# Kernel optimization log

Measured on AMD Instinct MI355X. Metric: run time of the kernel, lower is better.

Reference implementation:

```python
import jax, jax.numpy as jnp
import numpy as np
import math

DIM = 2880
N_HEADS = 64
N_KV = 8
HEAD_DIM = 64
WINDOW = 128          # layer_id = 0 (even) -> sliding window active
BASE = 150000.0
INIT_CTX = 4096
SCALE = 32.0
NTK_ALPHA = 1.0
NTK_BETA = 32.0
EPS = 1e-5
SEQ = 1536
BATCH = 1
SM_SCALE = 1.0 / math.sqrt(HEAD_DIM)


def _rope_tables(seq_len):
    """YaRN (NTK-by-parts) cos/sin tables, half-split convention. [S, D/2]."""
    freq = BASE ** (np.arange(0, HEAD_DIM, 2, dtype=np.float32) / HEAD_DIM)
    concentration = 0.1 * math.log(SCALE) + 1.0
    d_half = HEAD_DIM / 2
    low = d_half * math.log(INIT_CTX / (NTK_BETA * 2 * math.pi)) / math.log(BASE)
    high = d_half * math.log(INIT_CTX / (NTK_ALPHA * 2 * math.pi)) / math.log(BASE)
    interpolation = 1.0 / (SCALE * freq)
    extrapolation = 1.0 / freq
    ramp = (np.arange(d_half, dtype=np.float32) - low) / (high - low)
    mask = 1.0 - np.clip(ramp, 0.0, 1.0)
    inv_freq = interpolation * (1.0 - mask) + extrapolation * mask
    t = np.arange(seq_len, dtype=np.float32)
    freqs = np.outer(t, inv_freq)
    return (jnp.asarray(np.cos(freqs) * concentration),
            jnp.asarray(np.sin(freqs) * concentration))


def _apply_rope(x, cos, sin):
    # x: [B, S, H, D]; cos/sin: [S, D/2]
    c = cos[None, :, None, :]
    s = sin[None, :, None, :]
    x1, x2 = jnp.split(x, 2, axis=-1)
    return jnp.concatenate([x1 * c - x2 * s, x2 * c + x1 * s], axis=-1)


def setup_inputs() -> dict:
    key = jax.random.key(0)
    ks = jax.random.split(key, 5)
    x = jax.random.normal(ks[0], (BATCH, SEQ, DIM), dtype=jnp.float32)
    sinks = jax.random.normal(ks[1], (N_HEADS,), dtype=jnp.float32)
    norm_w = jnp.ones((DIM,), dtype=jnp.float32)
    qkv_dim = HEAD_DIM * (N_HEADS + 2 * N_KV)  # 5120
    qkv_w = jax.random.normal(ks[2], (qkv_dim, DIM), dtype=jnp.float32) / math.sqrt(DIM)
    qkv_b = jnp.zeros((qkv_dim,), dtype=jnp.float32)
    out_w = jax.random.normal(ks[3], (DIM, N_HEADS * HEAD_DIM), dtype=jnp.float32) / math.sqrt(N_HEADS * HEAD_DIM)
    out_b = jnp.zeros((DIM,), dtype=jnp.float32)
    return {"x": x, "sinks": sinks, "norm_w": norm_w, "qkv_w": qkv_w,
            "qkv_b": qkv_b, "out_w": out_w, "out_b": out_b}


def reference(x, sinks, norm_w, qkv_w, qkv_b, out_w, out_b):
    B, S, _ = x.shape
    # RMSNorm
    t = x * jax.lax.rsqrt(jnp.mean(x * x, axis=-1, keepdims=True) + EPS) * norm_w
    # fused QKV projection
    qkv = t @ qkv_w.T + qkv_b
    q_dim = N_HEADS * HEAD_DIM
    kv_dim = N_KV * HEAD_DIM
    q = qkv[..., :q_dim].reshape(B, S, N_HEADS, HEAD_DIM)
    k = qkv[..., q_dim:q_dim + kv_dim].reshape(B, S, N_KV, HEAD_DIM)
    v = qkv[..., q_dim + kv_dim:].reshape(B, S, N_KV, HEAD_DIM)
    # YaRN RoPE
    cos, sin = _rope_tables(S)
    q = _apply_rope(q, cos, sin)
    k = _apply_rope(k, cos, sin)
    # GQA: group query heads per kv head
    G = N_HEADS // N_KV
    qg = q.reshape(B, S, N_KV, G, HEAD_DIM)
    scores = jnp.einsum('bqkgd,bskd->bkgqs', qg, k) * SM_SCALE  # [B,KV,G,Sq,Sk]
    # causal + sliding-window mask
    i = jnp.arange(S)[:, None]
    j = jnp.arange(S)[None, :]
    allowed = j <= i
    if WINDOW > 0:
        allowed = allowed & ((i - j) < WINDOW)
    scores = jnp.where(allowed, scores, -jnp.inf)
    # sink tokens: one extra learned logit per head in the softmax denominator
    sink = sinks.reshape(N_KV, G)[None, :, :, None, None]
    sink = jnp.broadcast_to(sink, (B, N_KV, G, S, 1))
    logits = jnp.concatenate([scores, sink], axis=-1)  # [B,KV,G,Sq,Sk+1]
    p = jax.nn.softmax(logits, axis=-1)[..., :S]        # drop sink column
    attn = jnp.einsum('bkgqs,bskd->bqkgd', p, v).reshape(B, S, N_HEADS * HEAD_DIM)
    return attn @ out_w.T + out_b
```

## Files before the change

kernel.cpp:

```cpp
#include <hip/hip_runtime.h>

typedef unsigned short u16;
typedef unsigned int u32;
typedef __bf16 bf16x8 __attribute__((ext_vector_type(8)));
typedef float f32x4 __attribute__((ext_vector_type(4)));

#define S_LEN 1536
#define DIM 2880
#define NQH 64
#define NKVH 8
#define HD 64
#define QKV_N 5120
#define QDIM 4096
#define KVDIM 512
#define WIN 128
#define SM_SCALE 0.125f

__device__ __forceinline__ u16 f2bf(float f) {
  union { float f; u32 u; } a; a.f = f;
  u32 u = a.u;
  u32 lsb = (u >> 16) & 1;
  u += 0x7fffu + lsb;
  return (u16)(u >> 16);
}
__device__ __forceinline__ u32 pk2bf(float a, float b) {
  return (u32)f2bf(a) | ((u32)f2bf(b) << 16);
}

#define GLOAD16(g, l) __builtin_amdgcn_global_load_lds( \
    (const __attribute__((address_space(1))) u32*)(g), \
    (__attribute__((address_space(3))) u32*)(l), 16, 0, 0)

__global__ void rope_tables(float* __restrict__ cosT, float* __restrict__ sinT) {
  int idx = blockIdx.x * blockDim.x + threadIdx.x;
  if (idx >= S_LEN * 32) return;
  int s = idx >> 5, d = idx & 31;
  const double TWO_PI = 6.283185307179586;
  double freq = pow(150000.0, (double)d / 32.0);
  double conc = 0.1 * log(32.0) + 1.0;
  double lb = log(150000.0);
  double low = 32.0 * log(4096.0 / (32.0 * TWO_PI)) / lb;
  double high = 32.0 * log(4096.0 / (1.0 * TWO_PI)) / lb;
  double interp = 1.0 / (32.0 * freq), extra = 1.0 / freq;
  double ramp = ((double)d - low) / (high - low);
  ramp = ramp < 0.0 ? 0.0 : (ramp > 1.0 ? 1.0 : ramp);
  double maskv = 1.0 - ramp;
  double invf = interp * (1.0 - maskv) + extra * maskv;
  double ang = (double)s * invf;
  cosT[idx] = (float)(cos(ang) * conc);
  sinT[idx] = (float)(sin(ang) * conc);
}

__global__ __launch_bounds__(256) void rmsnorm_bf16(
    const float* __restrict__ x, const float* __restrict__ wgt,
    u16* __restrict__ th) {
  int row = blockIdx.x;
  const float* xr = x + (size_t)row * DIM;
  float ss = 0.f;
  for (int i = threadIdx.x; i < DIM / 4; i += 256) {
    float4 v = *(const float4*)&xr[i * 4];
    ss += v.x * v.x + v.y * v.y + v.z * v.z + v.w * v.w;
  }
  for (int m = 32; m >= 1; m >>= 1) ss += __shfl_xor(ss, m);
  __shared__ float red[4];
  int lane = threadIdx.x & 63, w = threadIdx.x >> 6;
  if (lane == 0) red[w] = ss;
  __syncthreads();
  float tot = red[0] + red[1] + red[2] + red[3];
  float scale = rsqrtf(tot / (float)DIM + 1e-5f);
  for (int i = threadIdx.x; i < DIM / 4; i += 256) {
    float4 v = *(const float4*)&xr[i * 4];
    float4 g = *(const float4*)&wgt[i * 4];
    ushort4 hi;
    hi.x = f2bf(v.x * scale * g.x);
    hi.y = f2bf(v.y * scale * g.y);
    hi.z = f2bf(v.z * scale * g.z);
    hi.w = f2bf(v.w * scale * g.w);
    *(ushort4*)&th[(size_t)row * DIM + i * 4] = hi;
  }
}

__global__ __launch_bounds__(256) void conv2(
    const float* __restrict__ s1, u16* __restrict__ d1, long n1,
    const float* __restrict__ s2, u16* __restrict__ d2, long n2) {
  long idx = (long)blockIdx.x * 256 + threadIdx.x;
  const float* src; u16* dst; long i;
  if (idx < n1) { src = s1; dst = d1; i = idx; }
  else if (idx < n1 + n2) { src = s2; dst = d2; i = idx - n1; }
  else return;
  float4 v = *(const float4*)&src[i * 4];
  ushort4 h;
  h.x = f2bf(v.x); h.y = f2bf(v.y); h.z = f2bf(v.z); h.w = f2bf(v.w);
  *(ushort4*)&dst[i * 4] = h;
}


__global__ __launch_bounds__(256) void gemm_rope(
    const u16* __restrict__ A, const u16* __restrict__ B,
    const float* __restrict__ bias,
    const float* __restrict__ cosT, const float* __restrict__ sinT,
    u16* __restrict__ Qb, u16* __restrict__ Kb, u16* __restrict__ Vt) {
  __shared__ u16 As[3 * 2048];
  __shared__ u16 Bs[3 * 4096];
  const int K = DIM;
  const int t = threadIdx.x;
  const int lane = t & 63, w = t >> 6;

  const int nby = gridDim.y;
  const int nwg = gridDim.x * nby;
  int orig = blockIdx.x * nby + blockIdx.y;
  {
    int q = nwg >> 3, r = nwg & 7;
    int xcd = orig & 7, i = orig >> 3;
    orig = (xcd < r ? xcd * (q + 1) : r * (q + 1) + (xcd - r) * q) + i;
  }
  const int m0 = (orig % nby) * 64, n0 = (orig / nby) * 128;

  const int wr = (w >> 1) * 32, wc = (w & 1) * 64;
  const int lr = lane & 15, lk8 = (lane >> 4) * 8;
  const int g4 = (lane >> 4) * 4;
  f32x4 acc[2][4] = {};

  const size_t ga  = (size_t)(m0 + (t >> 2)) * K + ((t & 3) * 8);
  const size_t gb0 = (size_t)(n0 + (t >> 2)) * K + ((t & 3) * 8);
  const size_t gb1 = (size_t)(n0 + 64 + (t >> 2)) * K + ((t & 3) * 8);
  const int la = t * 8, lb0 = t * 8, lb1 = (t + 256) * 8;

  auto STAGE = [&](int buf, int k0) {
    GLOAD16(A + ga + k0, &As[buf * 2048 + la]);
    GLOAD16(B + gb0 + k0, &Bs[buf * 4096 + lb0]);
    GLOAD16(B + gb1 + k0, &Bs[buf * 4096 + lb1]);
  };

  const int nk = K / 32;
  STAGE(0, 0); STAGE(1, 32);

  for (int tt = 0; tt < nk; ++tt) {
    const int cur = tt % 3;
    if (tt + 2 < nk) {
      STAGE((tt + 2) % 3, (tt + 2) * 32);
      asm volatile("s_waitcnt vmcnt(6)" ::: "memory");
    } else if (tt + 1 < nk) {
      asm volatile("s_waitcnt vmcnt(3)" ::: "memory");
    } else {
      asm volatile("s_waitcnt vmcnt(0)" ::: "memory");
    }
    __builtin_amdgcn_s_barrier();
    __builtin_amdgcn_sched_barrier(0);
    const u16* as_ = &As[cur * 2048];
    const u16* bs_ = &Bs[cur * 4096];
    bf16x8 af[2], bf_[4];
#pragma unroll
    for (int i = 0; i < 2; ++i) af[i] = *(const bf16x8*)&as_[(wr + i * 16 + lr) * 32 + lk8];
#pragma unroll
    for (int j = 0; j < 4; ++j) bf_[j] = *(const bf16x8*)&bs_[(wc + j * 16 + lr) * 32 + lk8];
#pragma unroll
    for (int i = 0; i < 2; ++i)
#pragma unroll
      for (int j = 0; j < 4; ++j)
        acc[i][j] = __builtin_amdgcn_mfma_f32_16x16x32_bf16(af[i], bf_[j], acc[i][j], 0, 0, 0);
    __builtin_amdgcn_sched_barrier(0);
    __builtin_amdgcn_s_barrier();
  }

  if (n0 < 4608) {
    const bool isQ = (n0 < 4096);
    const float sc = isQ ? SM_SCALE : 1.0f;
#pragma unroll
    for (int i = 0; i < 2; ++i) {
      const int row = m0 + wr + i * 16 + g4;
#pragma unroll
      for (int j = 0; j < 2; ++j) {
        const int col = n0 + wc + j * 16 + lr;
        const int d = j * 16 + lr;
        const float b1 = bias[col], b2 = bias[col + 32];
#pragma unroll
        for (int r = 0; r < 4; ++r) {
          const float c = cosT[(row + r) * 32 + d];
          const float s = sinT[(row + r) * 32 + d];
          const float x1 = acc[i][j][r] + b1;
          const float x2 = acc[i][j + 2][r] + b2;
          const float o1 = (x1 * c - x2 * s) * sc;
          const float o2 = (x2 * c + x1 * s) * sc;
          if (isQ) {
            Qb[(size_t)(row + r) * QDIM + col] = f2bf(o1);
            Qb[(size_t)(row + r) * QDIM + col + 32] = f2bf(o2);
          } else {
            Kb[(size_t)(row + r) * KVDIM + (col - 4096)] = f2bf(o1);
            Kb[(size_t)(row + r) * KVDIM + (col - 4096) + 32] = f2bf(o2);
          }
        }
      }
    }
  } else {
#pragma unroll
    for (int i = 0; i < 2; ++i) {
      const int rowb = m0 + wr + i * 16 + g4;
#pragma unroll
      for (int j = 0; j < 4; ++j) {
        const int col = n0 + wc + j * 16 + lr;
        const float bb = bias[col];
        ushort4 pk;
        pk.x = f2bf(acc[i][j][0] + bb);
        pk.y = f2bf(acc[i][j][1] + bb);
        pk.z = f2bf(acc[i][j][2] + bb);
        pk.w = f2bf(acc[i][j][3] + bb);
        *(ushort4*)&Vt[(size_t)(col - 4608) * S_LEN + rowb] = pk;
      }
    }
  }
}

__global__ __launch_bounds__(256) void gemm_bt(
    const u16* __restrict__ A, const u16* __restrict__ B,
    const float* __restrict__ bias, float* __restrict__ C,
    int M, int N, int K) {
  __shared__ u16 As[3 * 2048];
  __shared__ u16 Bs[3 * 4096];
  const int t = threadIdx.x;
  const int lane = t & 63, w = t >> 6;

  const int nby = gridDim.y;
  const int nwg = gridDim.x * nby;
  int orig = blockIdx.x * nby + blockIdx.y;
  {
    int q = nwg >> 3, r = nwg & 7;
    int xcd = orig & 7, i = orig >> 3;
    orig = (xcd < r ? xcd * (q + 1) : r * (q + 1) + (xcd - r) * q) + i;
  }
  const int m0 = (orig % nby) * 64, n0 = (orig / nby) * 128;

  const int wr = (w >> 1) * 32, wc = (w & 1) * 64;
  const int lr = lane & 15, lk8 = (lane >> 4) * 8;
  f32x4 acc[2][4] = {};

  int rB0 = n0 + (t >> 2); if (rB0 > N - 1) rB0 = N - 1;
  int rB1 = n0 + 64 + (t >> 2); if (rB1 > N - 1) rB1 = N - 1;
  const size_t ga  = (size_t)(m0 + (t >> 2)) * K + ((t & 3) * 8);
  const size_t gb0 = (size_t)rB0 * K + ((t & 3) * 8);
  const size_t gb1 = (size_t)rB1 * K + ((t & 3) * 8);
  const int la = t * 8, lb0 = t * 8, lb1 = (t + 256) * 8;

  auto STAGE = [&](int buf, int k0) {
    GLOAD16(A + ga + k0, &As[buf * 2048 + la]);
    GLOAD16(B + gb0 + k0, &Bs[buf * 4096 + lb0]);
    GLOAD16(B + gb1 + k0, &Bs[buf * 4096 + lb1]);
  };

  const int nk = K / 32;
  STAGE(0, 0); STAGE(1, 32);

  for (int tt = 0; tt < nk; ++tt) {
    const int cur = tt % 3;
    if (tt + 2 < nk) {
      STAGE((tt + 2) % 3, (tt + 2) * 32);
      asm volatile("s_waitcnt vmcnt(6)" ::: "memory");
    } else if (tt + 1 < nk) {
      asm volatile("s_waitcnt vmcnt(3)" ::: "memory");
    } else {
      asm volatile("s_waitcnt vmcnt(0)" ::: "memory");
    }
    __builtin_amdgcn_s_barrier();
    __builtin_amdgcn_sched_barrier(0);
    const u16* as_ = &As[cur * 2048];
    const u16* bs_ = &Bs[cur * 4096];
    bf16x8 af[2], bf_[4];
#pragma unroll
    for (int i = 0; i < 2; ++i) af[i] = *(const bf16x8*)&as_[(wr + i * 16 + lr) * 32 + lk8];
#pragma unroll
    for (int j = 0; j < 4; ++j) bf_[j] = *(const bf16x8*)&bs_[(wc + j * 16 + lr) * 32 + lk8];
#pragma unroll
    for (int i = 0; i < 2; ++i)
#pragma unroll
      for (int j = 0; j < 4; ++j)
        acc[i][j] = __builtin_amdgcn_mfma_f32_16x16x32_bf16(af[i], bf_[j], acc[i][j], 0, 0, 0);
    __builtin_amdgcn_sched_barrier(0);
    __builtin_amdgcn_s_barrier();
  }

#pragma unroll
  for (int i = 0; i < 2; ++i) {
    const int row = m0 + wr + i * 16 + (lane >> 4) * 4;
#pragma unroll
    for (int j = 0; j < 4; ++j) {
      const int col = n0 + wc + j * 16 + lr;
      if (col < N) {
        const float bb = bias[col];
#pragma unroll
        for (int r = 0; r < 4; ++r)
          C[(size_t)(row + r) * N + col] = acc[i][j][r] + bb;
      }
    }
  }
}

__global__ __launch_bounds__(256) void attn2(
    const u16* __restrict__ Q, const u16* __restrict__ Kb, const u16* __restrict__ Vt,
    const float* __restrict__ sinks, u16* __restrict__ O) {
  const int h = blockIdx.x;
  const int kh = h >> 3;
  const int wid = threadIdx.x >> 6;
  const int lane = threadIdx.x & 63;
  const int q0 = blockIdx.y * 128 + wid * 32;
  const int lr = lane & 15;
  const int g = lane >> 4;

  bf16x8 bq[2][2];
#pragma unroll
  for (int qf = 0; qf < 2; ++qf)
#pragma unroll
    for (int kc = 0; kc < 2; ++kc)
      bq[qf][kc] = *(const bf16x8*)&Q[(size_t)(q0 + qf * 16 + lr) * QDIM + h * HD + kc * 32 + g * 8];

  f32x4 o[2][4] = {};
  float m_s[2] = {-1e30f, -1e30f};
  float l_s[2] = {0.f, 0.f};

  int js = q0 - 128; if (js < 0) js = 0;

  for (int j0 = js; j0 <= q0; j0 += 32) {
    bf16x8 ak[2][2];
#pragma unroll
    for (int jf = 0; jf < 2; ++jf)
#pragma unroll
      for (int kc = 0; kc < 2; ++kc)
        ak[jf][kc] = *(const bf16x8*)&Kb[(size_t)(j0 + jf * 16 + lr) * KVDIM + kh * HD + kc * 32 + g * 8];

    f32x4 st[2][2] = {};
#pragma unroll
    for (int jf = 0; jf < 2; ++jf)
#pragma unroll
      for (int qf = 0; qf < 2; ++qf) {
        st[jf][qf] = __builtin_amdgcn_mfma_f32_16x16x32_bf16(ak[jf][0], bq[qf][0], st[jf][qf], 0, 0, 0);
        st[jf][qf] = __builtin_amdgcn_mfma_f32_16x16x32_bf16(ak[jf][1], bq[qf][1], st[jf][qf], 0, 0, 0);
      }

    float pv[2][2][4];
    float tmax[2] = {-1e30f, -1e30f};
#pragma unroll
    for (int jf = 0; jf < 2; ++jf)
#pragma unroll
      for (int qf = 0; qf < 2; ++qf)
#pragma unroll
        for (int r = 0; r < 4; ++r) {
          int jv = j0 + jf * 16 + 4 * g + r;
          int qq = q0 + qf * 16 + lr;
          float sc = st[jf][qf][r];
          bool ok = (jv <= qq) && (qq - jv < WIN);
          sc = ok ? sc : -1e30f;
          pv[jf][qf][r] = sc;
          tmax[qf] = fmaxf(tmax[qf], sc);
        }
#pragma unroll
    for (int qf = 0; qf < 2; ++qf) {
      float tm = tmax[qf];
      tm = fmaxf(tm, __shfl_xor(tm, 16));
      tm = fmaxf(tm, __shfl_xor(tm, 32));
      const float mo = m_s[qf];
      const float mn = fmaxf(mo, tm);
      const float esc = __expf(mo - mn);
      float ps = 0.f;
#pragma unroll
      for (int jf = 0; jf < 2; ++jf)
#pragma unroll
        for (int r = 0; r < 4; ++r) {
          float sv = pv[jf][qf][r];
          float e = __expf(sv - mn);
          e = (sv <= -1e29f) ? 0.f : e;
          pv[jf][qf][r] = e;
          ps += e;
        }
      ps += __shfl_xor(ps, 16);
      ps += __shfl_xor(ps, 32);
      l_s[qf] = l_s[qf] * esc + ps;
      m_s[qf] = mn;
#pragma unroll
      for (int df = 0; df < 4; ++df) o[qf][df] *= esc;
    }

    bf16x8 pb[2];
    const int srcA = lr + ((g & 1) ? 32 : 0);
    const int srcB = srcA + 16;
    const bool hi_half = (g >= 2);
#pragma unroll
    for (int qf = 0; qf < 2; ++qf) {
      u32 w0a = pk2bf(pv[0][qf][0], pv[0][qf][1]);
      u32 w1a = pk2bf(pv[0][qf][2], pv[0][qf][3]);
      u32 w0b = pk2bf(pv[1][qf][0], pv[1][qf][1]);
      u32 w1b = pk2bf(pv[1][qf][2], pv[1][qf][3]);
      u32 a0 = (u32)__shfl((int)w0a, srcA, 64);
      u32 a1 = (u32)__shfl((int)w1a, srcA, 64);
      u32 a2 = (u32)__shfl((int)w0a, srcB, 64);
      u32 a3 = (u32)__shfl((int)w1a, srcB, 64);
      u32 b0 = (u32)__shfl((int)w0b, srcA, 64);
      u32 b1 = (u32)__shfl((int)w1b, srcA, 64);
      u32 b2 = (u32)__shfl((int)w0b, srcB, 64);
      u32 b3 = (u32)__shfl((int)w1b, srcB, 64);
      union { u32 d[4]; bf16x8 v; } u_;
      u_.d[0] = hi_half ? b0 : a0;
      u_.d[1] = hi_half ? b1 : a1;
      u_.d[2] = hi_half ? b2 : a2;
      u_.d[3] = hi_half ? b3 : a3;
      pb[qf] = u_.v;
    }

    bf16x8 av[4];
#pragma unroll
    for (int df = 0; df < 4; ++df)
      av[df] = *(const bf16x8*)&Vt[((size_t)kh * HD + df * 16 + lr) * S_LEN + j0 + g * 8];

#pragma unroll
    for (int qf = 0; qf < 2; ++qf)
#pragma unroll
      for (int df = 0; df < 4; ++df)
        o[qf][df] = __builtin_amdgcn_mfma_f32_16x16x32_bf16(av[df], pb[qf], o[qf][df], 0, 0, 0);
  }

  const float snk = sinks[h];
#pragma unroll
  for (int qf = 0; qf < 2; ++qf) {
    const float mo = m_s[qf];
    const float Mx = fmaxf(mo, snk);
    const float den = l_s[qf] * __expf(mo - Mx) + __expf(snk - Mx);
    const float osc = __expf(mo - Mx) / den;
    const int row = q0 + qf * 16 + lr;
#pragma unroll
    for (int df = 0; df < 4; ++df) {
      ushort4 pk;
      pk.x = f2bf(o[qf][df][0] * osc);
      pk.y = f2bf(o[qf][df][1] * osc);
      pk.z = f2bf(o[qf][df][2] * osc);
      pk.w = f2bf(o[qf][df][3] * osc);
      *(ushort4*)&O[(size_t)row * QDIM + h * HD + df * 16 + 4 * g] = pk;
    }
  }
}

extern "C" void kernel_launch(void* const* d_in, const int* in_sizes, int n_in,
                              void* d_out, int out_size, void* d_ws, size_t ws_size,
                              hipStream_t stream) {
  const float* x      = (const float*)d_in[0];
  const float* sinks  = (const float*)d_in[1];
  const float* norm_w = (const float*)d_in[2];
  const float* qkv_w  = (const float*)d_in[3];
  const float* qkv_b  = (const float*)d_in[4];
  const float* out_w  = (const float*)d_in[5];
  const float* out_b  = (const float*)d_in[6];
  float* out = (float*)d_out;

  char* ws = (char*)d_ws;
  size_t off = 0;
  auto take = [&](size_t bytes) -> void* {
    void* r = ws + off;
    off += (bytes + 255) & ~(size_t)255;
    return r;
  };
  float* cosT = (float*)take((size_t)S_LEN * 32 * 4);
  float* sinT = (float*)take((size_t)S_LEN * 32 * 4);
  u16* th  = (u16*)take((size_t)S_LEN * DIM * 2);
  u16* wh  = (u16*)take((size_t)QKV_N * DIM * 2);
  u16* ow  = (u16*)take((size_t)DIM * QDIM * 2);
  u16* Qb  = (u16*)take((size_t)S_LEN * QDIM * 2);
  u16* Kb  = (u16*)take((size_t)S_LEN * KVDIM * 2);
  u16* Vt  = (u16*)take((size_t)S_LEN * KVDIM * 2);
  u16* Ab  = (u16*)take((size_t)S_LEN * QDIM * 2);

  const long n1 = (long)QKV_N * DIM / 4;
  const long n2 = (long)DIM * QDIM / 4;

  rope_tables<<<(S_LEN * 32 + 255) / 256, 256, 0, stream>>>(cosT, sinT);
  rmsnorm_bf16<<<S_LEN, 256, 0, stream>>>(x, norm_w, th);
  conv2<<<(int)((n1 + n2 + 255) / 256), 256, 0, stream>>>(qkv_w, wh, n1, out_w, ow, n2);
  gemm_rope<<<dim3(QKV_N / 128, S_LEN / 64), 256, 0, stream>>>(
      th, wh, qkv_b, cosT, sinT, Qb, Kb, Vt);
  attn2<<<dim3(NQH, S_LEN / 128), 256, 0, stream>>>(Qb, Kb, Vt, sinks, Ab);
  gemm_bt<<<dim3((DIM + 127) / 128, S_LEN / 64), 256, 0, stream>>>(
      Ab, ow, out_b, out, S_LEN, DIM, QDIM);
}
```

Baseline: 218.9 us.

## Use 2-wave GEMM blocks with 64x64 warp tiles and XOR-swizzled LDS

Both bf16 GEMMs (QKV+RoPE and output projection) drop from 4 waves to 2 waves per 64x128 block. Each wave now computes a 64x64 tile (4x4 MFMAs) instead of 32x64, which raises fragment reuse per LDS read. An XOR swizzle is applied to global-to-LDS placement and fragment reads to reduce LDS bank conflicts, and the waitcnt thresholds are adjusted for six loads per stage. The trade-off is fewer threads per block for latency hiding and higher accumulator register pressure.

```diff
diff --git a/kernel.cpp b/kernel.cpp
--- a/kernel.cpp
+++ b/kernel.cpp
@@ -95,7 +95,7 @@
 }
 
 
-__global__ __launch_bounds__(256) void gemm_rope(
+__global__ __launch_bounds__(128, 2) void gemm_rope(
     const u16* __restrict__ A, const u16* __restrict__ B,
     const float* __restrict__ bias,
     const float* __restrict__ cosT, const float* __restrict__ sinT,
@@ -116,20 +116,29 @@
   }
   const int m0 = (orig % nby) * 64, n0 = (orig / nby) * 128;
 
-  const int wr = (w >> 1) * 32, wc = (w & 1) * 64;
+  const int wc = w * 64;
   const int lr = lane & 15, lk8 = (lane >> 4) * 8;
+  const int lcol = lk8 ^ (((lr >> 1) & 3) << 3);
   const int g4 = (lane >> 4) * 4;
-  f32x4 acc[2][4] = {};
-
-  const size_t ga  = (size_t)(m0 + (t >> 2)) * K + ((t & 3) * 8);
-  const size_t gb0 = (size_t)(n0 + (t >> 2)) * K + ((t & 3) * 8);
-  const size_t gb1 = (size_t)(n0 + 64 + (t >> 2)) * K + ((t & 3) * 8);
-  const int la = t * 8, lb0 = t * 8, lb1 = (t + 256) * 8;
+  f32x4 acc[4][4] = {};
+
+  const int pA0 = t, pA1 = t + 128;
+  const size_t ga0 = (size_t)(m0 + (pA0 >> 2)) * K + (((pA0 & 3) ^ ((pA0 >> 3) & 3)) * 8);
+  const size_t ga1 = (size_t)(m0 + (pA1 >> 2)) * K + (((pA1 & 3) ^ ((pA1 >> 3) & 3)) * 8);
+  size_t gb[4];
+#pragma unroll
+  for (int c = 0; c < 4; ++c) {
+    const int p = t + c * 128;
+    gb[c] = (size_t)(n0 + (p >> 2)) * K + (((p & 3) ^ ((p >> 3) & 3)) * 8);
+  }
 
   auto STAGE = [&](int buf, int k0) {
-    GLOAD16(A + ga + k0, &As[buf * 2048 + la]);
-    GLOAD16(B + gb0 + k0, &Bs[buf * 4096 + lb0]);
-    GLOAD16(B + gb1 + k0, &Bs[buf * 4096 + lb1]);
+    GLOAD16(A + ga0 + k0, &As[buf * 2048 + t * 8]);
+    GLOAD16(A + ga1 + k0, &As[buf * 2048 + (t + 128) * 8]);
+    GLOAD16(B + gb[0] + k0, &Bs[buf * 4096 + t * 8]);
+    GLOAD16(B + gb[1] + k0, &Bs[buf * 4096 + (t + 128) * 8]);
+    GLOAD16(B + gb[2] + k0, &Bs[buf * 4096 + (t + 256) * 8]);
+    GLOAD16(B + gb[3] + k0, &Bs[buf * 4096 + (t + 384) * 8]);
   };
 
   const int nk = K / 32;
@@ -139,9 +148,9 @@
     const int cur = tt % 3;
     if (tt + 2 < nk) {
       STAGE((tt + 2) % 3, (tt + 2) * 32);
+      asm volatile("s_waitcnt vmcnt(12)" ::: "memory");
+    } else if (tt + 1 < nk) {
       asm volatile("s_waitcnt vmcnt(6)" ::: "memory");
-    } else if (tt + 1 < nk) {
-      asm volatile("s_waitcnt vmcnt(3)" ::: "memory");
     } else {
       asm volatile("s_waitcnt vmcnt(0)" ::: "memory");
     }
@@ -149,13 +158,13 @@
     __builtin_amdgcn_sched_barrier(0);
     const u16* as_ = &As[cur * 2048];
     const u16* bs_ = &Bs[cur * 4096];
-    bf16x8 af[2], bf_[4];
-#pragma unroll
-    for (int i = 0; i < 2; ++i) af[i] = *(const bf16x8*)&as_[(wr + i * 16 + lr) * 32 + lk8];
-#pragma unroll
-    for (int j = 0; j < 4; ++j) bf_[j] = *(const bf16x8*)&bs_[(wc + j * 16 + lr) * 32 + lk8];
-#pragma unroll
-    for (int i = 0; i < 2; ++i)
+    bf16x8 af[4], bf_[4];
+#pragma unroll
+    for (int i = 0; i < 4; ++i) af[i] = *(const bf16x8*)&as_[(i * 16 + lr) * 32 + lcol];
+#pragma unroll
+    for (int j = 0; j < 4; ++j) bf_[j] = *(const bf16x8*)&bs_[(wc + j * 16 + lr) * 32 + lcol];
+#pragma unroll
+    for (int i = 0; i < 4; ++i)
 #pragma unroll
       for (int j = 0; j < 4; ++j)
         acc[i][j] = __builtin_amdgcn_mfma_f32_16x16x32_bf16(af[i], bf_[j], acc[i][j], 0, 0, 0);
@@ -167,8 +176,8 @@
     const bool isQ = (n0 < 4096);
     const float sc = isQ ? SM_SCALE : 1.0f;
 #pragma unroll
-    for (int i = 0; i < 2; ++i) {
-      const int row = m0 + wr + i * 16 + g4;
+    for (int i = 0; i < 4; ++i) {
+      const int row = m0 + i * 16 + g4;
 #pragma unroll
       for (int j = 0; j < 2; ++j) {
         const int col = n0 + wc + j * 16 + lr;
@@ -194,8 +203,8 @@
     }
   } else {
 #pragma unroll
-    for (int i = 0; i < 2; ++i) {
-      const int rowb = m0 + wr + i * 16 + g4;
+    for (int i = 0; i < 4; ++i) {
+      const int rowb = m0 + i * 16 + g4;
 #pragma unroll
       for (int j = 0; j < 4; ++j) {
         const int col = n0 + wc + j * 16 + lr;
@@ -211,7 +220,7 @@
   }
 }
 
-__global__ __launch_bounds__(256) void gemm_bt(
+__global__ __launch_bounds__(128, 2) void gemm_bt(
     const u16* __restrict__ A, const u16* __restrict__ B,
     const float* __restrict__ bias, float* __restrict__ C,
     int M, int N, int K) {
@@ -230,21 +239,30 @@
   }
   const int m0 = (orig % nby) * 64, n0 = (orig / nby) * 128;
 
-  const int wr = (w >> 1) * 32, wc = (w & 1) * 64;
+  const int wc = w * 64;
   const int lr = lane & 15, lk8 = (lane >> 4) * 8;
-  f32x4 acc[2][4] = {};
-
-  int rB0 = n0 + (t >> 2); if (rB0 > N - 1) rB0 = N - 1;
-  int rB1 = n0 + 64 + (t >> 2); if (rB1 > N - 1) rB1 = N - 1;
-  const size_t ga  = (size_t)(m0 + (t >> 2)) * K + ((t & 3) * 8);
-  const size_t gb0 = (size_t)rB0 * K + ((t & 3) * 8);
-  const size_t gb1 = (size_t)rB1 * K + ((t & 3) * 8);
-  const int la = t * 8, lb0 = t * 8, lb1 = (t + 256) * 8;
+  const int lcol = lk8 ^ (((lr >> 1) & 3) << 3);
+  const int g4 = (lane >> 4) * 4;
+  f32x4 acc[4][4] = {};
+
+  const int pA0 = t, pA1 = t + 128;
+  const size_t ga0 = (size_t)(m0 + (pA0 >> 2)) * K + (((pA0 & 3) ^ ((pA0 >> 3) & 3)) * 8);
+  const size_t ga1 = (size_t)(m0 + (pA1 >> 2)) * K + (((pA1 & 3) ^ ((pA1 >> 3) & 3)) * 8);
+  size_t gb[4];
+#pragma unroll
+  for (int c = 0; c < 4; ++c) {
+    const int p = t + c * 128;
+    int rB = n0 + (p >> 2); if (rB > N - 1) rB = N - 1;
+    gb[c] = (size_t)rB * K + (((p & 3) ^ ((p >> 3) & 3)) * 8);
+  }
 
   auto STAGE = [&](int buf, int k0) {
-    GLOAD16(A + ga + k0, &As[buf * 2048 + la]);
-    GLOAD16(B + gb0 + k0, &Bs[buf * 4096 + lb0]);
-    GLOAD16(B + gb1 + k0, &Bs[buf * 4096 + lb1]);
+    GLOAD16(A + ga0 + k0, &As[buf * 2048 + t * 8]);
+    GLOAD16(A + ga1 + k0, &As[buf * 2048 + (t + 128) * 8]);
+    GLOAD16(B + gb[0] + k0, &Bs[buf * 4096 + t * 8]);
+    GLOAD16(B + gb[1] + k0, &Bs[buf * 4096 + (t + 128) * 8]);
+    GLOAD16(B + gb[2] + k0, &Bs[buf * 4096 + (t + 256) * 8]);
+    GLOAD16(B + gb[3] + k0, &Bs[buf * 4096 + (t + 384) * 8]);
   };
 
   const int nk = K / 32;
@@ -254,9 +272,9 @@
     const int cur = tt % 3;
     if (tt + 2 < nk) {
       STAGE((tt + 2) % 3, (tt + 2) * 32);
+      asm volatile("s_waitcnt vmcnt(12)" ::: "memory");
+    } else if (tt + 1 < nk) {
       asm volatile("s_waitcnt vmcnt(6)" ::: "memory");
-    } else if (tt + 1 < nk) {
-      asm volatile("s_waitcnt vmcnt(3)" ::: "memory");
     } else {
       asm volatile("s_waitcnt vmcnt(0)" ::: "memory");
     }
@@ -264,13 +282,13 @@
     __builtin_amdgcn_sched_barrier(0);
     const u16* as_ = &As[cur * 2048];
     const u16* bs_ = &Bs[cur * 4096];
-    bf16x8 af[2], bf_[4];
-#pragma unroll
-    for (int i = 0; i < 2; ++i) af[i] = *(const bf16x8*)&as_[(wr + i * 16 + lr) * 32 + lk8];
-#pragma unroll
-    for (int j = 0; j < 4; ++j) bf_[j] = *(const bf16x8*)&bs_[(wc + j * 16 + lr) * 32 + lk8];
-#pragma unroll
-    for (int i = 0; i < 2; ++i)
+    bf16x8 af[4], bf_[4];
+#pragma unroll
+    for (int i = 0; i < 4; ++i) af[i] = *(const bf16x8*)&as_[(i * 16 + lr) * 32 + lcol];
+#pragma unroll
+    for (int j = 0; j < 4; ++j) bf_[j] = *(const bf16x8*)&bs_[(wc + j * 16 + lr) * 32 + lcol];
+#pragma unroll
+    for (int i = 0; i < 4; ++i)
 #pragma unroll
       for (int j = 0; j < 4; ++j)
         acc[i][j] = __builtin_amdgcn_mfma_f32_16x16x32_bf16(af[i], bf_[j], acc[i][j], 0, 0, 0);
@@ -279,8 +297,8 @@
   }
 
 #pragma unroll
-  for (int i = 0; i < 2; ++i) {
-    const int row = m0 + wr + i * 16 + (lane >> 4) * 4;
+  for (int i = 0; i < 4; ++i) {
+    const int row = m0 + i * 16 + g4;
 #pragma unroll
     for (int j = 0; j < 4; ++j) {
       const int col = n0 + wc + j * 16 + lr;
@@ -471,9 +489,9 @@
   rope_tables<<<(S_LEN * 32 + 255) / 256, 256, 0, stream>>>(cosT, sinT);
   rmsnorm_bf16<<<S_LEN, 256, 0, stream>>>(x, norm_w, th);
   conv2<<<(int)((n1 + n2 + 255) / 256), 256, 0, stream>>>(qkv_w, wh, n1, out_w, ow, n2);
-  gemm_rope<<<dim3(QKV_N / 128, S_LEN / 64), 256, 0, stream>>>(
+  gemm_rope<<<dim3(QKV_N / 128, S_LEN / 64), 128, 0, stream>>>(
       th, wh, qkv_b, cosT, sinT, Qb, Kb, Vt);
   attn2<<<dim3(NQH, S_LEN / 128), 256, 0, stream>>>(Qb, Kb, Vt, sinks, Ab);
-  gemm_bt<<<dim3((DIM + 127) / 128, S_LEN / 64), 256, 0, stream>>>(
+  gemm_bt<<<dim3((DIM + 127) / 128, S_LEN / 64), 128, 0, stream>>>(
       Ab, ow, out_b, out, S_LEN, DIM, QDIM);
 }
```

After: 226.1 us. 3.3% more time.

## Use BK=64 double-buffered tiles with XOR-swizzled LDS in both GEMMs

Applied to the files above, without the earlier changes.

Both bf16 GEMMs move from a triple-buffered K=32 pipeline to a double-buffered K=64 pipeline. This halves the number of barrier pairs per tile, and each step issues 16 MFMAs instead of 8. Global-to-LDS loads permute the 16-byte chunks with an XOR swizzle, and the fragment reads apply the matching swizzle to reduce LDS bank conflicts. Launch bounds now request 3 blocks per CU. The trade-off is a shallower prefetch depth (one stage ahead instead of two) and more LDS per block.

```diff
diff --git a/kernel.cpp b/kernel.cpp
--- a/kernel.cpp
+++ b/kernel.cpp
@@ -95,13 +95,13 @@
 }
 
 
-__global__ __launch_bounds__(256) void gemm_rope(
+__global__ __launch_bounds__(256, 3) void gemm_rope(
     const u16* __restrict__ A, const u16* __restrict__ B,
     const float* __restrict__ bias,
     const float* __restrict__ cosT, const float* __restrict__ sinT,
     u16* __restrict__ Qb, u16* __restrict__ Kb, u16* __restrict__ Vt) {
-  __shared__ u16 As[3 * 2048];
-  __shared__ u16 Bs[3 * 4096];
+  __shared__ u16 As[2 * 4096];
+  __shared__ u16 Bs[2 * 8192];
   const int K = DIM;
   const int t = threadIdx.x;
   const int lane = t & 63, w = t >> 6;
@@ -118,47 +118,55 @@
 
   const int wr = (w >> 1) * 32, wc = (w & 1) * 64;
   const int lr = lane & 15, lk8 = (lane >> 4) * 8;
+  const int lcol = lk8 ^ (((lr >> 1) & 3) << 3);
   const int g4 = (lane >> 4) * 4;
   f32x4 acc[2][4] = {};
 
-  const size_t ga  = (size_t)(m0 + (t >> 2)) * K + ((t & 3) * 8);
-  const size_t gb0 = (size_t)(n0 + (t >> 2)) * K + ((t & 3) * 8);
-  const size_t gb1 = (size_t)(n0 + 64 + (t >> 2)) * K + ((t & 3) * 8);
-  const int la = t * 8, lb0 = t * 8, lb1 = (t + 256) * 8;
+  const size_t ga  = (size_t)(m0 + (t >> 2)) * K + (((t & 3) ^ ((t >> 3) & 3)) * 8);
+  const size_t gb0 = (size_t)(n0 + (t >> 2)) * K + (((t & 3) ^ ((t >> 3) & 3)) * 8);
+  const size_t gb1 = (size_t)(n0 + 64 + (t >> 2)) * K + (((t & 3) ^ ((t >> 3) & 3)) * 8);
 
   auto STAGE = [&](int buf, int k0) {
-    GLOAD16(A + ga + k0, &As[buf * 2048 + la]);
-    GLOAD16(B + gb0 + k0, &Bs[buf * 4096 + lb0]);
-    GLOAD16(B + gb1 + k0, &Bs[buf * 4096 + lb1]);
+    GLOAD16(A + ga + k0,        &As[buf * 4096 + t * 8]);
+    GLOAD16(A + ga + k0 + 32,   &As[buf * 4096 + 2048 + t * 8]);
+    GLOAD16(B + gb0 + k0,       &Bs[buf * 8192 + t * 8]);
+    GLOAD16(B + gb1 + k0,       &Bs[buf * 8192 + (t + 256) * 8]);
+    GLOAD16(B + gb0 + k0 + 32,  &Bs[buf * 8192 + 4096 + t * 8]);
+    GLOAD16(B + gb1 + k0 + 32,  &Bs[buf * 8192 + 4096 + (t + 256) * 8]);
   };
 
-  const int nk = K / 32;
-  STAGE(0, 0); STAGE(1, 32);
-
-  for (int tt = 0; tt < nk; ++tt) {
-    const int cur = tt % 3;
-    if (tt + 2 < nk) {
-      STAGE((tt + 2) % 3, (tt + 2) * 32);
+  const int nk2 = K / 64;
+  STAGE(0, 0);
+
+  for (int tt = 0; tt < nk2; ++tt) {
+    const int cur = tt & 1;
+    if (tt + 1 < nk2) {
+      STAGE(cur ^ 1, (tt + 1) * 64);
       asm volatile("s_waitcnt vmcnt(6)" ::: "memory");
-    } else if (tt + 1 < nk) {
-      asm volatile("s_waitcnt vmcnt(3)" ::: "memory");
     } else {
       asm volatile("s_waitcnt vmcnt(0)" ::: "memory");
     }
     __builtin_amdgcn_s_barrier();
     __builtin_amdgcn_sched_barrier(0);
-    const u16* as_ = &As[cur * 2048];
-    const u16* bs_ = &Bs[cur * 4096];
-    bf16x8 af[2], bf_[4];
-#pragma unroll
-    for (int i = 0; i < 2; ++i) af[i] = *(const bf16x8*)&as_[(wr + i * 16 + lr) * 32 + lk8];
-#pragma unroll
-    for (int j = 0; j < 4; ++j) bf_[j] = *(const bf16x8*)&bs_[(wc + j * 16 + lr) * 32 + lk8];
-#pragma unroll
-    for (int i = 0; i < 2; ++i)
+    const u16* as_ = &As[cur * 4096];
+    const u16* bs_ = &Bs[cur * 8192];
+    bf16x8 af[2][2], bf_[2][4];
+#pragma unroll
+    for (int ks = 0; ks < 2; ++ks) {
+#pragma unroll
+      for (int i = 0; i < 2; ++i)
+        af[ks][i] = *(const bf16x8*)&as_[ks * 2048 + (wr + i * 16 + lr) * 32 + lcol];
 #pragma unroll
       for (int j = 0; j < 4; ++j)
-        acc[i][j] = __builtin_amdgcn_mfma_f32_16x16x32_bf16(af[i], bf_[j], acc[i][j], 0, 0, 0);
+        bf_[ks][j] = *(const bf16x8*)&bs_[ks * 4096 + (wc + j * 16 + lr) * 32 + lcol];
+    }
+#pragma unroll
+    for (int ks = 0; ks < 2; ++ks)
+#pragma unroll
+      for (int i = 0; i < 2; ++i)
+#pragma unroll
+        for (int j = 0; j < 4; ++j)
+          acc[i][j] = __builtin_amdgcn_mfma_f32_16x16x32_bf16(af[ks][i], bf_[ks][j], acc[i][j], 0, 0, 0);
     __builtin_amdgcn_sched_barrier(0);
     __builtin_amdgcn_s_barrier();
   }
@@ -211,12 +219,12 @@
   }
 }
 
-__global__ __launch_bounds__(256) void gemm_bt(
+__global__ __launch_bounds__(256, 3) void gemm_bt(
     const u16* __restrict__ A, const u16* __restrict__ B,
     const float* __restrict__ bias, float* __restrict__ C,
     int M, int N, int K) {
-  __shared__ u16 As[3 * 2048];
-  __shared__ u16 Bs[3 * 4096];
+  __shared__ u16 As[2 * 4096];
+  __shared__ u16 Bs[2 * 8192];
   const int t = threadIdx.x;
   const int lane = t & 63, w = t >> 6;
 
@@ -232,55 +240,64 @@
 
   const int wr = (w >> 1) * 32, wc = (w & 1) * 64;
   const int lr = lane & 15, lk8 = (lane >> 4) * 8;
+  const int lcol = lk8 ^ (((lr >> 1) & 3) << 3);
+  const int g4 = (lane >> 4) * 4;
   f32x4 acc[2][4] = {};
 
   int rB0 = n0 + (t >> 2); if (rB0 > N - 1) rB0 = N - 1;
   int rB1 = n0 + 64 + (t >> 2); if (rB1 > N - 1) rB1 = N - 1;
-  const size_t ga  = (size_t)(m0 + (t >> 2)) * K + ((t & 3) * 8);
-  const size_t gb0 = (size_t)rB0 * K + ((t & 3) * 8);
-  const size_t gb1 = (size_t)rB1 * K + ((t & 3) * 8);
-  const int la = t * 8, lb0 = t * 8, lb1 = (t + 256) * 8;
+  const size_t ga  = (size_t)(m0 + (t >> 2)) * K + (((t & 3) ^ ((t >> 3) & 3)) * 8);
+  const size_t gb0 = (size_t)rB0 * K + (((t & 3) ^ ((t >> 3) & 3)) * 8);
+  const size_t gb1 = (size_t)rB1 * K + (((t & 3) ^ ((t >> 3) & 3)) * 8);
 
   auto STAGE = [&](int buf, int k0) {
-    GLOAD16(A + ga + k0, &As[buf * 2048 + la]);
-    GLOAD16(B + gb0 + k0, &Bs[buf * 4096 + lb0]);
-    GLOAD16(B + gb1 + k0, &Bs[buf * 4096 + lb1]);
+    GLOAD16(A + ga + k0,        &As[buf * 4096 + t * 8]);
+    GLOAD16(A + ga + k0 + 32,   &As[buf * 4096 + 2048 + t * 8]);
+    GLOAD16(B + gb0 + k0,       &Bs[buf * 8192 + t * 8]);
+    GLOAD16(B + gb1 + k0,       &Bs[buf * 8192 + (t + 256) * 8]);
+    GLOAD16(B + gb0 + k0 + 32,  &Bs[buf * 8192 + 4096 + t * 8]);
+    GLOAD16(B + gb1 + k0 + 32,  &Bs[buf * 8192 + 4096 + (t + 256) * 8]);
   };
 
-  const int nk = K / 32;
-  STAGE(0, 0); STAGE(1, 32);
-
-  for (int tt = 0; tt < nk; ++tt) {
-    const int cur = tt % 3;
-    if (tt + 2 < nk) {
-      STAGE((tt + 2) % 3, (tt + 2) * 32);
+  const int nk2 = K / 64;
+  STAGE(0, 0);
+
+  for (int tt = 0; tt < nk2; ++tt) {
+    const int cur = tt & 1;
+    if (tt + 1 < nk2) {
+      STAGE(cur ^ 1, (tt + 1) * 64);
       asm volatile("s_waitcnt vmcnt(6)" ::: "memory");
-    } else if (tt + 1 < nk) {
-      asm volatile("s_waitcnt vmcnt(3)" ::: "memory");
     } else {
       asm volatile("s_waitcnt vmcnt(0)" ::: "memory");
     }
     __builtin_amdgcn_s_barrier();
     __builtin_amdgcn_sched_barrier(0);
-    const u16* as_ = &As[cur * 2048];
-    const u16* bs_ = &Bs[cur * 4096];
-    bf16x8 af[2], bf_[4];
-#pragma unroll
-    for (int i = 0; i < 2; ++i) af[i] = *(const bf16x8*)&as_[(wr + i * 16 + lr) * 32 + lk8];
-#pragma unroll
-    for (int j = 0; j < 4; ++j) bf_[j] = *(const bf16x8*)&bs_[(wc + j * 16 + lr) * 32 + lk8];
-#pragma unroll
-    for (int i = 0; i < 2; ++i)
+    const u16* as_ = &As[cur * 4096];
+    const u16* bs_ = &Bs[cur * 8192];
+    bf16x8 af[2][2], bf_[2][4];
+#pragma unroll
+    for (int ks = 0; ks < 2; ++ks) {
+#pragma unroll
+      for (int i = 0; i < 2; ++i)
+        af[ks][i] = *(const bf16x8*)&as_[ks * 2048 + (wr + i * 16 + lr) * 32 + lcol];
 #pragma unroll
       for (int j = 0; j < 4; ++j)
-        acc[i][j] = __builtin_amdgcn_mfma_f32_16x16x32_bf16(af[i], bf_[j], acc[i][j], 0, 0, 0);
+        bf_[ks][j] = *(const bf16x8*)&bs_[ks * 4096 + (wc + j * 16 + lr) * 32 + lcol];
+    }
+#pragma unroll
+    for (int ks = 0; ks < 2; ++ks)
+#pragma unroll
+      for (int i = 0; i < 2; ++i)
+#pragma unroll
+        for (int j = 0; j < 4; ++j)
+          acc[i][j] = __builtin_amdgcn_mfma_f32_16x16x32_bf16(af[ks][i], bf_[ks][j], acc[i][j], 0, 0, 0);
     __builtin_amdgcn_sched_barrier(0);
     __builtin_amdgcn_s_barrier();
   }
 
 #pragma unroll
   for (int i = 0; i < 2; ++i) {
-    const int row = m0 + wr + i * 16 + (lane >> 4) * 4;
+    const int row = m0 + wr + i * 16 + g4;
 #pragma unroll
     for (int j = 0; j < 4; ++j) {
       const int col = n0 + wc + j * 16 + lr;
```

Measured after the change: 207.7 us. 1.05x faster.

## Swizzle GEMM LDS layout, single barrier per k-step, add setprio and occupancy hint

Applied to the files above, without the earlier changes.

Both GEMM kernels now XOR-swizzle the k-chunk columns when loading global data into LDS and read fragments through the matching swizzled column, to reduce LDS bank conflicts. The loop drops the trailing barrier and issues the next-next stage after the leading barrier, so each k-step needs one barrier instead of two. MFMA blocks are wrapped in s_setprio, and launch_bounds requests four blocks per SIMD. The vmcnt accounting is changed to match the new issue order; if the wait counts or swizzle mapping are off, the result is wrong or the loop stalls.

```diff
diff --git a/kernel.cpp b/kernel.cpp
--- a/kernel.cpp
+++ b/kernel.cpp
@@ -95,7 +95,7 @@
 }
 
 
-__global__ __launch_bounds__(256) void gemm_rope(
+__global__ __launch_bounds__(256, 4) void gemm_rope(
     const u16* __restrict__ A, const u16* __restrict__ B,
     const float* __restrict__ bias,
     const float* __restrict__ cosT, const float* __restrict__ sinT,
@@ -118,18 +118,18 @@
 
   const int wr = (w >> 1) * 32, wc = (w & 1) * 64;
   const int lr = lane & 15, lk8 = (lane >> 4) * 8;
+  const int lcol = lk8 ^ (((lr >> 1) & 3) << 3);
   const int g4 = (lane >> 4) * 4;
   f32x4 acc[2][4] = {};
 
-  const size_t ga  = (size_t)(m0 + (t >> 2)) * K + ((t & 3) * 8);
-  const size_t gb0 = (size_t)(n0 + (t >> 2)) * K + ((t & 3) * 8);
-  const size_t gb1 = (size_t)(n0 + 64 + (t >> 2)) * K + ((t & 3) * 8);
-  const int la = t * 8, lb0 = t * 8, lb1 = (t + 256) * 8;
+  const size_t ga  = (size_t)(m0 + (t >> 2)) * K + (((t & 3) ^ ((t >> 3) & 3)) * 8);
+  const size_t gb0 = (size_t)(n0 + (t >> 2)) * K + (((t & 3) ^ ((t >> 3) & 3)) * 8);
+  const size_t gb1 = (size_t)(n0 + 64 + (t >> 2)) * K + (((t & 3) ^ ((t >> 3) & 3)) * 8);
 
   auto STAGE = [&](int buf, int k0) {
-    GLOAD16(A + ga + k0, &As[buf * 2048 + la]);
-    GLOAD16(B + gb0 + k0, &Bs[buf * 4096 + lb0]);
-    GLOAD16(B + gb1 + k0, &Bs[buf * 4096 + lb1]);
+    GLOAD16(A + ga + k0,  &As[buf * 2048 + t * 8]);
+    GLOAD16(B + gb0 + k0, &Bs[buf * 4096 + t * 8]);
+    GLOAD16(B + gb1 + k0, &Bs[buf * 4096 + (t + 256) * 8]);
   };
 
   const int nk = K / 32;
@@ -137,30 +137,28 @@
 
   for (int tt = 0; tt < nk; ++tt) {
     const int cur = tt % 3;
-    if (tt + 2 < nk) {
-      STAGE((tt + 2) % 3, (tt + 2) * 32);
+    if (tt + 1 < nk) {
       asm volatile("s_waitcnt vmcnt(6)" ::: "memory");
-    } else if (tt + 1 < nk) {
-      asm volatile("s_waitcnt vmcnt(3)" ::: "memory");
     } else {
       asm volatile("s_waitcnt vmcnt(0)" ::: "memory");
     }
     __builtin_amdgcn_s_barrier();
     __builtin_amdgcn_sched_barrier(0);
+    if (tt + 2 < nk) STAGE((tt + 2) % 3, (tt + 2) * 32);
     const u16* as_ = &As[cur * 2048];
     const u16* bs_ = &Bs[cur * 4096];
     bf16x8 af[2], bf_[4];
 #pragma unroll
-    for (int i = 0; i < 2; ++i) af[i] = *(const bf16x8*)&as_[(wr + i * 16 + lr) * 32 + lk8];
-#pragma unroll
-    for (int j = 0; j < 4; ++j) bf_[j] = *(const bf16x8*)&bs_[(wc + j * 16 + lr) * 32 + lk8];
+    for (int i = 0; i < 2; ++i) af[i] = *(const bf16x8*)&as_[(wr + i * 16 + lr) * 32 + lcol];
+#pragma unroll
+    for (int j = 0; j < 4; ++j) bf_[j] = *(const bf16x8*)&bs_[(wc + j * 16 + lr) * 32 + lcol];
+    __builtin_amdgcn_s_setprio(1);
 #pragma unroll
     for (int i = 0; i < 2; ++i)
 #pragma unroll
       for (int j = 0; j < 4; ++j)
         acc[i][j] = __builtin_amdgcn_mfma_f32_16x16x32_bf16(af[i], bf_[j], acc[i][j], 0, 0, 0);
-    __builtin_amdgcn_sched_barrier(0);
-    __builtin_amdgcn_s_barrier();
+    __builtin_amdgcn_s_setprio(0);
   }
 
   if (n0 < 4608) {
@@ -211,7 +209,7 @@
   }
 }
 
-__global__ __launch_bounds__(256) void gemm_bt(
+__global__ __launch_bounds__(256, 4) void gemm_bt(
     const u16* __restrict__ A, const u16* __restrict__ B,
     const float* __restrict__ bias, float* __restrict__ C,
     int M, int N, int K) {
@@ -232,19 +230,20 @@
 
   const int wr = (w >> 1) * 32, wc = (w & 1) * 64;
   const int lr = lane & 15, lk8 = (lane >> 4) * 8;
+  const int lcol = lk8 ^ (((lr >> 1) & 3) << 3);
+  const int g4 = (lane >> 4) * 4;
   f32x4 acc[2][4] = {};
 
   int rB0 = n0 + (t >> 2); if (rB0 > N - 1) rB0 = N - 1;
   int rB1 = n0 + 64 + (t >> 2); if (rB1 > N - 1) rB1 = N - 1;
-  const size_t ga  = (size_t)(m0 + (t >> 2)) * K + ((t & 3) * 8);
-  const size_t gb0 = (size_t)rB0 * K + ((t & 3) * 8);
-  const size_t gb1 = (size_t)rB1 * K + ((t & 3) * 8);
-  const int la = t * 8, lb0 = t * 8, lb1 = (t + 256) * 8;
+  const size_t ga  = (size_t)(m0 + (t >> 2)) * K + (((t & 3) ^ ((t >> 3) & 3)) * 8);
+  const size_t gb0 = (size_t)rB0 * K + (((t & 3) ^ ((t >> 3) & 3)) * 8);
+  const size_t gb1 = (size_t)rB1 * K + (((t & 3) ^ ((t >> 3) & 3)) * 8);
 
   auto STAGE = [&](int buf, int k0) {
-    GLOAD16(A + ga + k0, &As[buf * 2048 + la]);
-    GLOAD16(B + gb0 + k0, &Bs[buf * 4096 + lb0]);
-    GLOAD16(B + gb1 + k0, &Bs[buf * 4096 + lb1]);
+    GLOAD16(A + ga + k0,  &As[buf * 2048 + t * 8]);
+    GLOAD16(B + gb0 + k0, &Bs[buf * 4096 + t * 8]);
+    GLOAD16(B + gb1 + k0, &Bs[buf * 4096 + (t + 256) * 8]);
   };
 
   const int nk = K / 32;
@@ -252,35 +251,33 @@
 
   for (int tt = 0; tt < nk; ++tt) {
     const int cur = tt % 3;
-    if (tt + 2 < nk) {
-      STAGE((tt + 2) % 3, (tt + 2) * 32);
+    if (tt + 1 < nk) {
       asm volatile("s_waitcnt vmcnt(6)" ::: "memory");
-    } else if (tt + 1 < nk) {
-      asm volatile("s_waitcnt vmcnt(3)" ::: "memory");
     } else {
       asm volatile("s_waitcnt vmcnt(0)" ::: "memory");
     }
     __builtin_amdgcn_s_barrier();
     __builtin_amdgcn_sched_barrier(0);
+    if (tt + 2 < nk) STAGE((tt + 2) % 3, (tt + 2) * 32);
     const u16* as_ = &As[cur * 2048];
     const u16* bs_ = &Bs[cur * 4096];
     bf16x8 af[2], bf_[4];
 #pragma unroll
-    for (int i = 0; i < 2; ++i) af[i] = *(const bf16x8*)&as_[(wr + i * 16 + lr) * 32 + lk8];
-#pragma unroll
-    for (int j = 0; j < 4; ++j) bf_[j] = *(const bf16x8*)&bs_[(wc + j * 16 + lr) * 32 + lk8];
+    for (int i = 0; i < 2; ++i) af[i] = *(const bf16x8*)&as_[(wr + i * 16 + lr) * 32 + lcol];
+#pragma unroll
+    for (int j = 0; j < 4; ++j) bf_[j] = *(const bf16x8*)&bs_[(wc + j * 16 + lr) * 32 + lcol];
+    __builtin_amdgcn_s_setprio(1);
 #pragma unroll
     for (int i = 0; i < 2; ++i)
 #pragma unroll
       for (int j = 0; j < 4; ++j)
         acc[i][j] = __builtin_amdgcn_mfma_f32_16x16x32_bf16(af[i], bf_[j], acc[i][j], 0, 0, 0);
-    __builtin_amdgcn_sched_barrier(0);
-    __builtin_amdgcn_s_barrier();
+    __builtin_amdgcn_s_setprio(0);
   }
 
 #pragma unroll
   for (int i = 0; i < 2; ++i) {
-    const int row = m0 + wr + i * 16 + (lane >> 4) * 4;
+    const int row = m0 + wr + i * 16 + g4;
 #pragma unroll
     for (int j = 0; j < 4; ++j) {
       const int col = n0 + wc + j * 16 + lr;
```

Result: no change. 216.6 us (-1.1%).
